# Performance work log

Measured on AMD Instinct MI355X. Metric: run time of the kernel, lower is better.

Reference implementation:

```python
import jax, jax.numpy as jnp
import numpy as np

N, E, K, IN_C, D = 50000, 800000, 3, 2, 64
RES_LAYERS = 2
EPS = 1e-5


def setup_inputs() -> dict:
    key = jax.random.key(0)
    ks = jax.random.split(key, 12)
    def w(k, shape, scale=0.05):
        return jax.random.normal(k, shape, jnp.float32) * scale
    x = jax.random.normal(ks[0], (N, IN_C), jnp.float32)
    edge_index = jax.random.randint(ks[1], (2, E), 0, N, dtype=jnp.int32)
    edge_attr = jax.random.uniform(ks[2], (E,), jnp.float32)
    # TAGConv params: first conv IN_C->D, then 2*RES_LAYERS + 1 = 5 convs D->D, each with K+1 weight mats
    tag0_w = w(ks[3], (K + 1, IN_C, D))
    tag0_b = jnp.zeros((D,), jnp.float32)
    tag_w = w(ks[4], (5, K + 1, D, D))
    tag_b = jnp.zeros((5, D), jnp.float32)
    # EdgeModel params: Lin(2D+1,D) + 2 residual blocks (Lin,ReLU,Lin)+LN + Lin(D,1)
    We0 = w(ks[5], (2 * D + 1, D)); be0 = jnp.zeros((D,), jnp.float32)
    ln0_g = jnp.ones((D,), jnp.float32); ln0_b = jnp.zeros((D,), jnp.float32)
    Wa = w(ks[6], (2, D, D)); ba = jnp.zeros((2, D), jnp.float32)
    Wb = w(ks[7], (2, D, D)); bb = jnp.zeros((2, D), jnp.float32)
    ln_g = jnp.ones((2, D), jnp.float32); ln_b = jnp.zeros((2, D), jnp.float32)
    Wf = w(ks[8], (D, 1)); bf = jnp.zeros((1,), jnp.float32)
    return dict(x=x, edge_index=edge_index, edge_attr=edge_attr,
                tag0_w=tag0_w, tag0_b=tag0_b, tag_w=tag_w, tag_b=tag_b,
                We0=We0, be0=be0, ln0_g=ln0_g, ln0_b=ln0_b,
                Wa=Wa, ba=ba, Wb=Wb, bb=bb, ln_g=ln_g, ln_b=ln_b,
                Wf=Wf, bf=bf)


def _gcn_norm(row, col, ew, n):
    # symmetric GCN normalization without self loops (PyG TAGConv default)
    deg = jnp.zeros((n,), ew.dtype).at[col].add(ew)
    deg_safe = jnp.where(deg > 0, deg, 1.0)
    dinv = jnp.where(deg > 0, jax.lax.rsqrt(deg_safe), 0.0)
    return dinv[row] * ew * dinv[col]


def _tagconv(x, row, col, norm, W, b):
    # out = sum_{k=0..K} (A_norm^k x) @ W[k] + b
    out = x @ W[0]
    h = x
    for k in range(1, K + 1):
        h = jnp.zeros(h.shape, h.dtype).at[col].add(norm[:, None] * h[row])
        out = out + h @ W[k]
    return out + b


def _inorm(x):
    # PyG InstanceNorm, single graph, affine=False: per-channel stats over nodes
    m = x.mean(0)
    v = x.var(0)
    return (x - m) * jax.lax.rsqrt(v + EPS)


def _lnorm(x, g, b):
    m = x.mean(-1, keepdims=True)
    v = x.var(-1, keepdims=True)
    return (x - m) * jax.lax.rsqrt(v + EPS) * g + b


def _forward(x, edge_index, edge_attr, tag0_w, tag0_b, tag_w, tag_b,
             We0, be0, ln0_g, ln0_b, Wa, ba, Wb, bb, ln_g, ln_b, Wf, bf):
    row, col = edge_index[0], edge_index[1]
    ew = edge_attr.reshape(-1)
    norm = _gcn_norm(row, col, ew, x.shape[0])
    # block 0: TAGConv(IN_C->D) -> InstanceNorm -> (no residual: shape change) -> ReLU
    data = jax.nn.relu(_inorm(_tagconv(x, row, col, norm, tag0_w, tag0_b)))
    # residual blocks: TAGConv -> ReLU -> TAGConv -> InstanceNorm -> +residual -> ReLU
    for i in range(RES_LAYERS):
        h = jax.nn.relu(_tagconv(data, row, col, norm, tag_w[2 * i], tag_b[2 * i]))
        h = _inorm(_tagconv(h, row, col, norm, tag_w[2 * i + 1], tag_b[2 * i + 1]))
        data = jax.nn.relu(h + data)
    # final block: TAGConv -> (no norm) -> +residual -> ReLU
    data = jax.nn.relu(_tagconv(data, row, col, norm, tag_w[4], tag_b[4]) + data)
    # edge model on gathered endpoint features + edge attr
    e = jnp.concatenate([data[row], data[col], ew[:, None]], axis=1)  # [E, 2D+1]
    h = jax.nn.relu(_lnorm(e @ We0 + be0, ln0_g, ln0_b))  # no residual (shape change)
    for j in range(2):
        h2 = jax.nn.relu(h @ Wa[j] + ba[j]) @ Wb[j] + bb[j]
        h = jax.nn.relu(_lnorm(h2, ln_g[j], ln_b[j]) + h)
    out = h @ Wf + bf  # [E, 1]
    out = (out - out.mean()) / out.std(ddof=1)
    return jnp.abs(out)


def reference(x, edge_index, edge_attr, tag0_w, tag0_b, tag_w, tag_b,
              We0, be0, ln0_g, ln0_b, Wa, ba, Wb, bb, ln_g, ln_b, Wf, bf):
    return _forward(x, edge_index, edge_attr, tag0_w, tag0_b, tag_w, tag_b,
                    We0, be0, ln0_g, ln0_b, Wa, ba, Wb, bb, ln_g, ln_b, Wf, bf)
```

## Files before the change

kernel.cpp:

```cpp
#include <hip/hip_runtime.h>

#define NN 50000
#define NE 800000
#define EPSf 1e-5f

typedef _Float16 half8 __attribute__((ext_vector_type(8)));
typedef _Float16 half4v __attribute__((ext_vector_type(4)));
typedef _Float16 half2v __attribute__((ext_vector_type(2)));
typedef float f32x4 __attribute__((ext_vector_type(4)));

#define HA_STRIDE 72
#define WT_STRIDE 136
#define WB_STRIDE 72

__global__ void deg_hist_kernel(const int* __restrict__ row, const int* __restrict__ col,
                                const float* __restrict__ ew,
                                float* __restrict__ deg, int* __restrict__ cnt) {
  int e = blockIdx.x * 256 + threadIdx.x;
  if (e >= NE) return;
  int c = col[e];
  unsafeAtomicAdd(&deg[c], ew[e]);
  atomicAdd(&cnt[c], 1);
}

__global__ void dinv_kernel(float* __restrict__ deg) {
  int n = blockIdx.x * 256 + threadIdx.x;
  if (n >= NN) return;
  float d = deg[n];
  deg[n] = d > 0.f ? rsqrtf(d) : 0.f;
}

__global__ void scan1(int* __restrict__ cnt, int* __restrict__ aux) {
  __shared__ int ls[256];
  int t = threadIdx.x, idx = blockIdx.x * 256 + t;
  int v = (idx < NN) ? cnt[idx] : 0;
  ls[t] = v;
  __syncthreads();
  for (int o = 1; o < 256; o <<= 1) {
    int u = (t >= o) ? ls[t - o] : 0;
    __syncthreads();
    ls[t] += u;
    __syncthreads();
  }
  if (idx < NN) cnt[idx] = ls[t] - v;
  if (t == 255) aux[blockIdx.x] = ls[255];
}

__global__ void scan2(int* __restrict__ aux, int nb) {
  __shared__ int ls[256];
  int t = threadIdx.x;
  int v = (t < nb) ? aux[t] : 0;
  ls[t] = v;
  __syncthreads();
  for (int o = 1; o < 256; o <<= 1) {
    int u = (t >= o) ? ls[t - o] : 0;
    __syncthreads();
    ls[t] += u;
    __syncthreads();
  }
  if (t < nb) aux[t] = ls[t] - v;
}

__global__ void scan3(int* __restrict__ cnt, const int* __restrict__ aux) {
  int idx = blockIdx.x * 256 + threadIdx.x;
  if (idx < NN) cnt[idx] += aux[idx >> 8];
}

__global__ void scatter_kernel(const int* __restrict__ row, const int* __restrict__ col,
                               const float* __restrict__ ew, const float* __restrict__ dinv,
                               int* __restrict__ rowptr, int2* __restrict__ pme) {
  int e = blockIdx.x * 256 + threadIdx.x;
  if (e >= NE) return;
  int r = row[e], c = col[e];
  float w = dinv[r] * ew[e] * dinv[c];
  int p = atomicAdd(&rowptr[c], 1);
  pme[p] = make_int2(r, __float_as_int(w));
}

__global__ void prop16(const int* __restrict__ rowptr, const int2* __restrict__ pme,
                       const _Float16* __restrict__ h, _Float16* __restrict__ hn) {
  int idx = blockIdx.x * 256 + threadIdx.x;
  if (idx >= NN * 8) return;
  int n = idx >> 3, q = idx & 7;
  int s = n ? rowptr[n - 1] : 0;
  int epos = rowptr[n];
  float a0 = 0.f, a1 = 0.f, a2 = 0.f, a3 = 0.f, a4 = 0.f, a5 = 0.f, a6 = 0.f, a7 = 0.f;
  for (int j = s; j < epos; j++) {
    int2 m = pme[j];
    float w = __int_as_float(m.y);
    half8 v = *(const half8*)&h[(size_t)m.x * 64 + q * 8];
    a0 += w * (float)v[0]; a1 += w * (float)v[1];
    a2 += w * (float)v[2]; a3 += w * (float)v[3];
    a4 += w * (float)v[4]; a5 += w * (float)v[5];
    a6 += w * (float)v[6]; a7 += w * (float)v[7];
  }
  half8 o = {(_Float16)a0, (_Float16)a1, (_Float16)a2, (_Float16)a3,
             (_Float16)a4, (_Float16)a5, (_Float16)a6, (_Float16)a7};
  *(half8*)&hn[(size_t)n * 64 + q * 8] = o;
}

__global__ void prop2_csr(const int* __restrict__ rowptr, const int2* __restrict__ pme,
                          const float* __restrict__ h, float* __restrict__ hn) {
  int n = blockIdx.x * 256 + threadIdx.x;
  if (n >= NN) return;
  int s = n ? rowptr[n - 1] : 0;
  int epos = rowptr[n];
  float a0 = 0.f, a1 = 0.f;
  for (int j = s; j < epos; j++) {
    int2 m = pme[j];
    float w = __int_as_float(m.y);
    a0 += w * h[m.x * 2 + 0];
    a1 += w * h[m.x * 2 + 1];
  }
  hn[n * 2 + 0] = a0;
  hn[n * 2 + 1] = a1;
}

__global__ void __launch_bounds__(128, 4) gemmB_mfma(
    const _Float16* __restrict__ h0, const _Float16* __restrict__ h1,
    const _Float16* __restrict__ h2, const _Float16* __restrict__ h3,
    const float* __restrict__ W,
    float* __restrict__ accG) {
  __shared__ __align__(16) _Float16 hA[128 * HA_STRIDE];
  __shared__ __align__(16) _Float16 WT[64 * WB_STRIDE];
  const int t = threadIdx.x;
  const int lane = t & 63, wv = t >> 6;
  const int a = lane & 15, g = lane >> 4;
  const int nb = blockIdx.x * 128;
  const _Float16* hs[4] = {h0, h1, h2, h3};

  f32x4 acc[4][4];
#pragma unroll
  for (int ct = 0; ct < 4; ct++)
#pragma unroll
    for (int nt = 0; nt < 4; nt++) acc[ct][nt] = (f32x4)0.f;

#pragma unroll 1
  for (int k = 0; k < 4; k++) {
    const _Float16* hk = hs[k];
    {
      size_t base = (size_t)(nb + t) * 64;
#pragma unroll
      for (int i = 0; i < 8; i++)
        *(half8*)&hA[t * HA_STRIDE + i * 8] = *(const half8*)&hk[base + i * 8];
    }
    {
      const float* Wk = W + k * 4096;
      int n = t >> 1, kb = (t & 1) * 32;
#pragma unroll
      for (int k2 = 0; k2 < 16; k2++) {
        int kk = kb + 2 * k2;
        half2v p = {(_Float16)Wk[kk * 64 + n], (_Float16)Wk[(kk + 1) * 64 + n]};
        *(half2v*)&WT[n * WB_STRIDE + kk] = p;
      }
    }
    __syncthreads();
#pragma unroll
    for (int ks = 0; ks < 2; ks++) {
      half8 wf[4], hf[4];
#pragma unroll
      for (int nt = 0; nt < 4; nt++)
        wf[nt] = *(const half8*)&WT[(nt * 16 + a) * WB_STRIDE + ks * 32 + g * 8];
#pragma unroll
      for (int ct = 0; ct < 4; ct++)
        hf[ct] = *(const half8*)&hA[(wv * 64 + ct * 16 + a) * HA_STRIDE + ks * 32 + g * 8];
#pragma unroll
      for (int ct = 0; ct < 4; ct++)
#pragma unroll
        for (int nt = 0; nt < 4; nt++)
          acc[ct][nt] = __builtin_amdgcn_mfma_f32_16x16x32_f16(wf[nt], hf[ct], acc[ct][nt], 0, 0, 0);
    }
    __syncthreads();
  }
#pragma unroll
  for (int ct = 0; ct < 4; ct++) {
    int node = nb + wv * 64 + ct * 16 + a;
    if (node < NN) {
#pragma unroll
      for (int nt = 0; nt < 4; nt++)
        *(f32x4*)&accG[(size_t)node * 64 + nt * 16 + g * 4] = acc[ct][nt];
    }
  }
}

__global__ void gemm2(const float* __restrict__ h2, const float* __restrict__ W,
                      float* __restrict__ acc, int accum) {
  int idx = blockIdx.x * 256 + threadIdx.x;
  if (idx >= NN * 16) return;
  int n = idx >> 4, q = idx & 15;
  float x0 = h2[n * 2], x1 = h2[n * 2 + 1];
  float4 w0 = ((const float4*)W)[q];
  float4 w1 = ((const float4*)W)[16 + q];
  float4 a;
  if (accum) a = ((const float4*)acc)[idx];
  else a = make_float4(0.f, 0.f, 0.f, 0.f);
  a.x += x0 * w0.x + x1 * w1.x;
  a.y += x0 * w0.y + x1 * w1.y;
  a.z += x0 * w0.z + x1 * w1.z;
  a.w += x0 * w0.w + x1 * w1.w;
  ((float4*)acc)[idx] = a;
}

__global__ void stats64(const float* __restrict__ acc, float* __restrict__ st) {
  int c = threadIdx.x & 63, g = threadIdx.x >> 6;
  float s = 0.f, ss = 0.f;
  for (int n = blockIdx.x * 4 + g; n < NN; n += gridDim.x * 4) {
    float v = acc[n * 64 + c];
    s += v; ss += v * v;
  }
  __shared__ float ls[256], lss[256];
  ls[threadIdx.x] = s; lss[threadIdx.x] = ss;
  __syncthreads();
  if (threadIdx.x < 64) {
    s = ls[threadIdx.x] + ls[threadIdx.x + 64] + ls[threadIdx.x + 128] + ls[threadIdx.x + 192];
    ss = lss[threadIdx.x] + lss[threadIdx.x + 64] + lss[threadIdx.x + 128] + lss[threadIdx.x + 192];
    unsafeAtomicAdd(&st[c], s);
    unsafeAtomicAdd(&st[64 + c], ss);
  }
}

__global__ void apply64(const float* __restrict__ acc, const float* __restrict__ bias,
                        const float* __restrict__ st, const float* __restrict__ resid,
                        float* __restrict__ out32, _Float16* __restrict__ out16,
                        int inorm, int relu) {
  int idx = blockIdx.x * 256 + threadIdx.x;
  if (idx >= NN * 16) return;
  int q = idx & 15;
  int c0 = q * 4;
  const float4 av = ((const float4*)acc)[idx];
  float v0 = av.x, v1 = av.y, v2 = av.z, v3 = av.w;
  if (inorm) {
    const float invN = 1.f / NN;
    float m0 = st[c0 + 0] * invN, m1 = st[c0 + 1] * invN;
    float m2 = st[c0 + 2] * invN, m3 = st[c0 + 3] * invN;
    float r0 = rsqrtf(st[64 + c0 + 0] * invN - m0 * m0 + EPSf);
    float r1 = rsqrtf(st[64 + c0 + 1] * invN - m1 * m1 + EPSf);
    float r2 = rsqrtf(st[64 + c0 + 2] * invN - m2 * m2 + EPSf);
    float r3 = rsqrtf(st[64 + c0 + 3] * invN - m3 * m3 + EPSf);
    v0 = (v0 - m0) * r0; v1 = (v1 - m1) * r1;
    v2 = (v2 - m2) * r2; v3 = (v3 - m3) * r3;
  } else {
    v0 += bias[c0 + 0]; v1 += bias[c0 + 1]; v2 += bias[c0 + 2]; v3 += bias[c0 + 3];
  }
  if (resid) {
    const float4 rv = ((const float4*)resid)[idx];
    v0 += rv.x; v1 += rv.y; v2 += rv.z; v3 += rv.w;
  }
  if (relu) {
    v0 = fmaxf(v0, 0.f); v1 = fmaxf(v1, 0.f);
    v2 = fmaxf(v2, 0.f); v3 = fmaxf(v3, 0.f);
  }
  if (out32) ((float4*)out32)[idx] = make_float4(v0, v1, v2, v3);
  if (out16) {
    half4v hh = {(_Float16)v0, (_Float16)v1, (_Float16)v2, (_Float16)v3};
    *(half4v*)&out16[(size_t)idx * 4] = hh;
  }
}

__device__ __forceinline__ void gemm64_step(f32x4 (&acc)[4][4],
                                            const _Float16* hAp, const _Float16* WTp,
                                            int wv, int a, int g, int koff) {
#pragma unroll
  for (int ks = 0; ks < 2; ks++) {
    half8 wf[4], hf[4];
#pragma unroll
    for (int nt = 0; nt < 4; nt++)
      wf[nt] = *(const half8*)&WTp[(nt * 16 + a) * WT_STRIDE + koff + ks * 32 + g * 8];
#pragma unroll
    for (int ct = 0; ct < 4; ct++)
      hf[ct] = *(const half8*)&hAp[(wv * 64 + ct * 16 + a) * HA_STRIDE + ks * 32 + g * 8];
#pragma unroll
    for (int ct = 0; ct < 4; ct++)
#pragma unroll
      for (int nt = 0; nt < 4; nt++)
        acc[ct][nt] = __builtin_amdgcn_mfma_f32_16x16x32_f16(wf[nt], hf[ct], acc[ct][nt], 0, 0, 0);
  }
}

__global__ void __launch_bounds__(256, 2) edge_mlp_mfma(
    const _Float16* __restrict__ dat16, const int* __restrict__ row, const int* __restrict__ col,
    const float* __restrict__ ew,
    const float* __restrict__ We0, const float* __restrict__ be0,
    const float* __restrict__ g0, const float* __restrict__ b0,
    const float* __restrict__ Wa, const float* __restrict__ ba,
    const float* __restrict__ Wb, const float* __restrict__ bb,
    const float* __restrict__ lg, const float* __restrict__ lb,
    const float* __restrict__ Wf, const float* __restrict__ bfp,
    float* __restrict__ eout) {
  __shared__ __align__(16) _Float16 hA[256 * HA_STRIDE];
  __shared__ __align__(16) _Float16 WT[64 * WT_STRIDE];
  __shared__ float sew[256];

  const int t = threadIdx.x;
  const int lane = t & 63, wv = t >> 6;
  const int a = lane & 15, g = lane >> 4;
  const int eb = blockIdx.x * 256;

  {
    int e = eb + t;
    sew[t] = ew[e];
    int r = row[e];
    const _Float16* srcp = dat16 + (size_t)r * 64;
#pragma unroll
    for (int i = 0; i < 8; i++)
      *(half8*)&hA[t * HA_STRIDE + i * 8] = *(const half8*)&srcp[i * 8];
    int n = t >> 2, kb = (t & 3) * 32;
#pragma unroll
    for (int k2 = 0; k2 < 16; k2++) {
      int k = kb + 2 * k2;
      half2v p = {(_Float16)We0[k * 64 + n], (_Float16)We0[(k + 1) * 64 + n]};
      *(half2v*)&WT[n * WT_STRIDE + k] = p;
    }
  }

  f32x4 be0v[4], w128v[4], g0v[4], b0v[4];
#pragma unroll
  for (int nt = 0; nt < 4; nt++) {
    int ch = nt * 16 + g * 4;
    be0v[nt] = *(const f32x4*)&be0[ch];
    w128v[nt] = *(const f32x4*)&We0[128 * 64 + ch];
    g0v[nt] = *(const f32x4*)&g0[ch];
    b0v[nt] = *(const f32x4*)&b0[ch];
  }

  __syncthreads();

  f32x4 acc[4][4];
#pragma unroll
  for (int ct = 0; ct < 4; ct++) {
    float we = sew[wv * 64 + ct * 16 + a];
#pragma unroll
    for (int nt = 0; nt < 4; nt++) acc[ct][nt] = be0v[nt] + we * w128v[nt];
  }
  gemm64_step(acc, hA, WT, wv, a, g, 0);
  __syncthreads();
  {
    int e = eb + t;
    int c = col[e];
    const _Float16* srcp = dat16 + (size_t)c * 64;
#pragma unroll
    for (int i = 0; i < 8; i++)
      *(half8*)&hA[t * HA_STRIDE + i * 8] = *(const half8*)&srcp[i * 8];
  }
  __syncthreads();
  gemm64_step(acc, hA, WT, wv, a, g, 64);

  f32x4 h[4][4];
#pragma unroll
  for (int ct = 0; ct < 4; ct++) {
    float s = 0.f, ss = 0.f;
#pragma unroll
    for (int nt = 0; nt < 4; nt++)
#pragma unroll
      for (int r = 0; r < 4; r++) { float v = acc[ct][nt][r]; s += v; ss += v * v; }
    s += __shfl_xor(s, 16); ss += __shfl_xor(ss, 16);
    s += __shfl_xor(s, 32); ss += __shfl_xor(ss, 32);
    float m = s * (1.f / 64);
    float is = rsqrtf(ss * (1.f / 64) - m * m + EPSf);
#pragma unroll
    for (int nt = 0; nt < 4; nt++)
#pragma unroll
      for (int r = 0; r < 4; r++)
        h[ct][nt][r] = fmaxf((acc[ct][nt][r] - m) * is * g0v[nt][r] + b0v[nt][r], 0.f);
  }
  __syncthreads();

#pragma unroll 1
  for (int j = 0; j < 2; j++) {
    {
      const float* W = Wa + j * 4096;
      int n = t >> 2, kb = (t & 3) * 16;
#pragma unroll
      for (int k2 = 0; k2 < 8; k2++) {
        int k = kb + 2 * k2;
        half2v p = {(_Float16)W[k * 64 + n], (_Float16)W[(k + 1) * 64 + n]};
        *(half2v*)&WT[n * WT_STRIDE + k] = p;
      }
    }
#pragma unroll
    for (int ct = 0; ct < 4; ct++)
#pragma unroll
      for (int nt = 0; nt < 4; nt++) {
        half4v hh = {(_Float16)h[ct][nt][0], (_Float16)h[ct][nt][1],
                     (_Float16)h[ct][nt][2], (_Float16)h[ct][nt][3]};
        *(half4v*)&hA[(wv * 64 + ct * 16 + a) * HA_STRIDE + nt * 16 + g * 4] = hh;
      }
    __syncthreads();
    f32x4 accT[4][4];
#pragma unroll
    for (int nt = 0; nt < 4; nt++) {
      f32x4 bv = *(const f32x4*)&ba[j * 64 + nt * 16 + g * 4];
#pragma unroll
      for (int ct = 0; ct < 4; ct++) accT[ct][nt] = bv;
    }
    gemm64_step(accT, hA, WT, wv, a, g, 0);
    __syncthreads();
    {
      const float* W = Wb + j * 4096;
      int n = t >> 2, kb = (t & 3) * 16;
#pragma unroll
      for (int k2 = 0; k2 < 8; k2++) {
        int k = kb + 2 * k2;
        half2v p = {(_Float16)W[k * 64 + n], (_Float16)W[(k + 1) * 64 + n]};
        *(half2v*)&WT[n * WT_STRIDE + k] = p;
      }
    }
#pragma unroll
    for (int ct = 0; ct < 4; ct++)
#pragma unroll
      for (int nt = 0; nt < 4; nt++) {
        half4v hh = {(_Float16)fmaxf(accT[ct][nt][0], 0.f), (_Float16)fmaxf(accT[ct][nt][1], 0.f),
                     (_Float16)fmaxf(accT[ct][nt][2], 0.f), (_Float16)fmaxf(accT[ct][nt][3], 0.f)};
        *(half4v*)&hA[(wv * 64 + ct * 16 + a) * HA_STRIDE + nt * 16 + g * 4] = hh;
      }
    __syncthreads();
    f32x4 accB[4][4];
#pragma unroll
    for (int nt = 0; nt < 4; nt++) {
      f32x4 bv = *(const f32x4*)&bb[j * 64 + nt * 16 + g * 4];
#pragma unroll
      for (int ct = 0; ct < 4; ct++) accB[ct][nt] = bv;
    }
    gemm64_step(accB, hA, WT, wv, a, g, 0);

    f32x4 lgv[4], lbv[4];
#pragma unroll
    for (int nt = 0; nt < 4; nt++) {
      lgv[nt] = *(const f32x4*)&lg[j * 64 + nt * 16 + g * 4];
      lbv[nt] = *(const f32x4*)&lb[j * 64 + nt * 16 + g * 4];
    }
#pragma unroll
    for (int ct = 0; ct < 4; ct++) {
      float s = 0.f, ss = 0.f;
#pragma unroll
      for (int nt = 0; nt < 4; nt++)
#pragma unroll
        for (int r = 0; r < 4; r++) { float v = accB[ct][nt][r]; s += v; ss += v * v; }
      s += __shfl_xor(s, 16); ss += __shfl_xor(ss, 16);
      s += __shfl_xor(s, 32); ss += __shfl_xor(ss, 32);
      float m = s * (1.f / 64);
      float is = rsqrtf(ss * (1.f / 64) - m * m + EPSf);
#pragma unroll
      for (int nt = 0; nt < 4; nt++)
#pragma unroll
        for (int r = 0; r < 4; r++)
          h[ct][nt][r] =
              fmaxf((accB[ct][nt][r] - m) * is * lgv[nt][r] + lbv[nt][r] + h[ct][nt][r], 0.f);
    }
    __syncthreads();
  }

  f32x4 wfv[4];
#pragma unroll
  for (int nt = 0; nt < 4; nt++) wfv[nt] = *(const f32x4*)&Wf[nt * 16 + g * 4];
  float p0 = 0.f, p1 = 0.f, p2 = 0.f, p3 = 0.f;
#pragma unroll
  for (int nt = 0; nt < 4; nt++)
#pragma unroll
    for (int r = 0; r < 4; r++) {
      p0 += h[0][nt][r] * wfv[nt][r];
      p1 += h[1][nt][r] * wfv[nt][r];
      p2 += h[2][nt][r] * wfv[nt][r];
      p3 += h[3][nt][r] * wfv[nt][r];
    }
  p0 += __shfl_xor(p0, 16); p0 += __shfl_xor(p0, 32);
  p1 += __shfl_xor(p1, 16); p1 += __shfl_xor(p1, 32);
  p2 += __shfl_xor(p2, 16); p2 += __shfl_xor(p2, 32);
  p3 += __shfl_xor(p3, 16); p3 += __shfl_xor(p3, 32);
  float sel = (g == 0) ? p0 : (g == 1) ? p1 : (g == 2) ? p2 : p3;
  eout[eb + t] = sel + bfp[0];
}

__global__ void reduce2(const float* __restrict__ v, float* __restrict__ est) {
  __shared__ float ls[256], lss[256];
  float s = 0.f, ss = 0.f;
  for (int i = blockIdx.x * 256 + threadIdx.x; i < NE; i += gridDim.x * 256) {
    float a = v[i]; s += a; ss += a * a;
  }
  ls[threadIdx.x] = s; lss[threadIdx.x] = ss;
  __syncthreads();
  for (int o = 128; o > 0; o >>= 1) {
    if (threadIdx.x < o) { ls[threadIdx.x] += ls[threadIdx.x + o]; lss[threadIdx.x] += lss[threadIdx.x + o]; }
    __syncthreads();
  }
  if (threadIdx.x == 0) {
    unsafeAtomicAdd(&est[0], ls[0]);
    unsafeAtomicAdd(&est[1], lss[0]);
  }
}

__global__ void finalize(const float* __restrict__ eo, const float* __restrict__ est,
                         float* __restrict__ out) {
  int e = blockIdx.x * 256 + threadIdx.x;
  if (e >= NE) return;
  float sum = est[0], ssq = est[1];
  float m = sum * (1.f / NE);
  float var = (ssq - sum * sum * (1.f / NE)) * (1.f / (NE - 1));
  out[e] = fabsf((eo[e] - m) * rsqrtf(var));
}

extern "C" void kernel_launch(void* const* d_in, const int* in_sizes, int n_in,
                              void* d_out, int out_size, void* d_ws, size_t ws_size,
                              hipStream_t stream) {
  const float* x   = (const float*)d_in[0];
  const int*   ei  = (const int*)d_in[1];
  const float* ew  = (const float*)d_in[2];
  const float* t0w = (const float*)d_in[3];
  const float* t0b = (const float*)d_in[4];
  const float* tw  = (const float*)d_in[5];
  const float* tb  = (const float*)d_in[6];
  const float* We0 = (const float*)d_in[7];
  const float* be0 = (const float*)d_in[8];
  const float* g0  = (const float*)d_in[9];
  const float* b0  = (const float*)d_in[10];
  const float* Wa  = (const float*)d_in[11];
  const float* ba  = (const float*)d_in[12];
  const float* Wb  = (const float*)d_in[13];
  const float* bb  = (const float*)d_in[14];
  const float* lg  = (const float*)d_in[15];
  const float* lb  = (const float*)d_in[16];
  const float* Wf  = (const float*)d_in[17];
  const float* bf  = (const float*)d_in[18];
  const int* row = ei;
  const int* col = ei + NE;

  float* ws = (float*)d_ws;
  int*       rowptr = (int*)ws;
  int2*      pme    = (int2*)(ws + 50048);
  float*     st     = ws + 1650048;
  float*     est    = st + 128;
  float*     acc    = ws + 1650240;
  float*     dat    = acc + 3200000;
  _Float16*  cur16  = (_Float16*)(ws + 8050240);
  _Float16*  mid16  = (_Float16*)(ws + 9650240);
  _Float16*  h1     = (_Float16*)(ws + 11250240);
  _Float16*  h2     = (_Float16*)(ws + 12850240);
  _Float16*  h3     = (_Float16*)(ws + 14450240);
  float*     eout   = ws + 16050240;
  float*     dinv   = ws + 11250240;
  int*       aux    = (int*)(ws + 12850240);
  float*     b2a    = ws + 14450240;
  float*     b2b    = b2a + 100096;

  dim3 blk(256);
#define GRID(n) dim3(((n) + 255) / 256)
  const int NB = (NN + 255) / 256;

  hipMemsetAsync(dinv, 0, NN * sizeof(float), stream);
  hipMemsetAsync(rowptr, 0, NN * sizeof(int), stream);
  deg_hist_kernel<<<GRID(NE), blk, 0, stream>>>(row, col, ew, dinv, rowptr);
  dinv_kernel<<<GRID(NN), blk, 0, stream>>>(dinv);
  scan1<<<dim3(NB), blk, 0, stream>>>(rowptr, aux);
  scan2<<<dim3(1), blk, 0, stream>>>(aux, NB);
  scan3<<<dim3(NB), blk, 0, stream>>>(rowptr, aux);
  scatter_kernel<<<GRID(NE), blk, 0, stream>>>(row, col, ew, dinv, rowptr, pme);

  gemm2<<<GRID(NN * 16), blk, 0, stream>>>(x, t0w, acc, 0);
  prop2_csr<<<dim3(NB), blk, 0, stream>>>(rowptr, pme, x, b2a);
  gemm2<<<GRID(NN * 16), blk, 0, stream>>>(b2a, t0w + 128, acc, 1);
  prop2_csr<<<dim3(NB), blk, 0, stream>>>(rowptr, pme, b2a, b2b);
  gemm2<<<GRID(NN * 16), blk, 0, stream>>>(b2b, t0w + 256, acc, 1);
  prop2_csr<<<dim3(NB), blk, 0, stream>>>(rowptr, pme, b2b, b2a);
  gemm2<<<GRID(NN * 16), blk, 0, stream>>>(b2a, t0w + 384, acc, 1);
  hipMemsetAsync(st, 0, 128 * sizeof(float), stream);
  stats64<<<dim3(128), blk, 0, stream>>>(acc, st);
  apply64<<<GRID(NN * 16), blk, 0, stream>>>(acc, t0b, st, nullptr, dat, cur16, 1, 1);

  const int GBB = (NN + 127) / 128;
  auto tag16 = [&](const _Float16* src, const float* W) {
    prop16<<<GRID(NN * 8), blk, 0, stream>>>(rowptr, pme, src, h1);
    prop16<<<GRID(NN * 8), blk, 0, stream>>>(rowptr, pme, h1, h2);
    prop16<<<GRID(NN * 8), blk, 0, stream>>>(rowptr, pme, h2, h3);
    gemmB_mfma<<<dim3(GBB), dim3(128), 0, stream>>>(src, h1, h2, h3, W, acc);
  };

  for (int i = 0; i < 2; i++) {
    tag16(cur16, tw + (2 * i) * 16384);
    apply64<<<GRID(NN * 16), blk, 0, stream>>>(acc, tb + (2 * i) * 64, nullptr, nullptr,
                                               nullptr, mid16, 0, 1);
    tag16(mid16, tw + (2 * i + 1) * 16384);
    hipMemsetAsync(st, 0, 128 * sizeof(float), stream);
    stats64<<<dim3(128), blk, 0, stream>>>(acc, st);
    apply64<<<GRID(NN * 16), blk, 0, stream>>>(acc, tb + (2 * i + 1) * 64, st, dat,
                                               dat, cur16, 1, 1);
  }
  tag16(cur16, tw + 4 * 16384);
  apply64<<<GRID(NN * 16), blk, 0, stream>>>(acc, tb + 4 * 64, nullptr, dat,
                                             nullptr, cur16, 0, 1);

  edge_mlp_mfma<<<GRID(NE), blk, 0, stream>>>(cur16, row, col, ew, We0, be0, g0, b0,
                                              Wa, ba, Wb, bb, lg, lb, Wf, bf, eout);
  hipMemsetAsync(est, 0, 2 * sizeof(float), stream);
  reduce2<<<dim3(1024), blk, 0, stream>>>(eout, est);
  finalize<<<GRID(NE), blk, 0, stream>>>(eout, est, (float*)d_out);
#undef GRID
}
```

Before: 886.7 us.

## Fuse TAGConv epilogues into MFMA GEMM, widen prop16, pre-convert edge-MLP weights

Bias, ReLU, residual and fp16 output are folded into the gemmB_mfma epilogue, and so are the instance-norm statistics via wave shuffles and atomics. This removes the separate apply64 and stats64 passes and one fp32 round-trip through memory. The first layer's three gemm2 launches become one gemm2B that reads all hop buffers at once. prop16 now has each thread handle 16 channels and unrolls edges by four, giving more loads in flight per thread. The edge-MLP weights are converted to transposed fp16 once in a small kernel and read straight from global memory instead of being staged into LDS in every block. The costs are global or cache weight reads inside the MFMA inner loop, more atomics on the statistics, and higher register pressure in prop16.

```diff
diff --git a/kernel.cpp b/kernel.cpp
--- a/kernel.cpp
+++ b/kernel.cpp
@@ -10,7 +10,6 @@
 typedef float f32x4 __attribute__((ext_vector_type(4)));
 
 #define HA_STRIDE 72
-#define WT_STRIDE 136
 #define WB_STRIDE 72
 
 __global__ void deg_hist_kernel(const int* __restrict__ row, const int* __restrict__ col,
@@ -77,26 +76,64 @@
   pme[p] = make_int2(r, __float_as_int(w));
 }
 
+__global__ void cvt_w(const float* __restrict__ We0, const float* __restrict__ Wa,
+                      const float* __restrict__ Wb, _Float16* __restrict__ wt) {
+  int i = blockIdx.x * 256 + threadIdx.x;
+  if (i < 8192) {
+    int n = i >> 7, k = i & 127;
+    wt[i] = (_Float16)We0[k * 64 + n];
+  } else if (i < 16384) {
+    int i2 = i - 8192, j = i2 >> 12, n = (i2 >> 6) & 63, k = i2 & 63;
+    wt[i] = (_Float16)Wa[j * 4096 + k * 64 + n];
+  } else if (i < 24576) {
+    int i2 = i - 16384, j = i2 >> 12, n = (i2 >> 6) & 63, k = i2 & 63;
+    wt[i] = (_Float16)Wb[j * 4096 + k * 64 + n];
+  }
+}
+
 __global__ void prop16(const int* __restrict__ rowptr, const int2* __restrict__ pme,
                        const _Float16* __restrict__ h, _Float16* __restrict__ hn) {
   int idx = blockIdx.x * 256 + threadIdx.x;
-  if (idx >= NN * 8) return;
-  int n = idx >> 3, q = idx & 7;
+  if (idx >= NN * 4) return;
+  int n = idx >> 2, q = idx & 3;
   int s = n ? rowptr[n - 1] : 0;
   int epos = rowptr[n];
-  float a0 = 0.f, a1 = 0.f, a2 = 0.f, a3 = 0.f, a4 = 0.f, a5 = 0.f, a6 = 0.f, a7 = 0.f;
-  for (int j = s; j < epos; j++) {
+  const _Float16* hq = h + q * 16;
+  float a[16];
+#pragma unroll
+  for (int i = 0; i < 16; i++) a[i] = 0.f;
+  int j = s;
+  for (; j + 4 <= epos; j += 4) {
+    int2 m0 = pme[j], m1 = pme[j + 1], m2 = pme[j + 2], m3 = pme[j + 3];
+    const half8* p0 = (const half8*)&hq[(size_t)m0.x * 64];
+    const half8* p1 = (const half8*)&hq[(size_t)m1.x * 64];
+    const half8* p2 = (const half8*)&hq[(size_t)m2.x * 64];
+    const half8* p3 = (const half8*)&hq[(size_t)m3.x * 64];
+    half8 u0 = p0[0], u1 = p0[1];
+    half8 u2 = p1[0], u3 = p1[1];
+    half8 u4 = p2[0], u5 = p2[1];
+    half8 u6 = p3[0], u7 = p3[1];
+    float w0 = __int_as_float(m0.y), w1 = __int_as_float(m1.y);
+    float w2 = __int_as_float(m2.y), w3 = __int_as_float(m3.y);
+#pragma unroll
+    for (int i = 0; i < 8; i++) {
+      a[i]     += w0 * (float)u0[i] + w1 * (float)u2[i] + w2 * (float)u4[i] + w3 * (float)u6[i];
+      a[i + 8] += w0 * (float)u1[i] + w1 * (float)u3[i] + w2 * (float)u5[i] + w3 * (float)u7[i];
+    }
+  }
+  for (; j < epos; j++) {
     int2 m = pme[j];
     float w = __int_as_float(m.y);
-    half8 v = *(const half8*)&h[(size_t)m.x * 64 + q * 8];
-    a0 += w * (float)v[0]; a1 += w * (float)v[1];
-    a2 += w * (float)v[2]; a3 += w * (float)v[3];
-    a4 += w * (float)v[4]; a5 += w * (float)v[5];
-    a6 += w * (float)v[6]; a7 += w * (float)v[7];
-  }
-  half8 o = {(_Float16)a0, (_Float16)a1, (_Float16)a2, (_Float16)a3,
-             (_Float16)a4, (_Float16)a5, (_Float16)a6, (_Float16)a7};
-  *(half8*)&hn[(size_t)n * 64 + q * 8] = o;
+    const half8* p = (const half8*)&hq[(size_t)m.x * 64];
+    half8 u0 = p[0], u1 = p[1];
+#pragma unroll
+    for (int i = 0; i < 8; i++) { a[i] += w * (float)u0[i]; a[i + 8] += w * (float)u1[i]; }
+  }
+  half8 o0, o1;
+#pragma unroll
+  for (int i = 0; i < 8; i++) { o0[i] = (_Float16)a[i]; o1[i] = (_Float16)a[i + 8]; }
+  *(half8*)&hn[(size_t)n * 64 + q * 16] = o0;
+  *(half8*)&hn[(size_t)n * 64 + q * 16 + 8] = o1;
 }
 
 __global__ void prop2_csr(const int* __restrict__ rowptr, const int2* __restrict__ pme,
@@ -120,7 +157,9 @@
     const _Float16* __restrict__ h0, const _Float16* __restrict__ h1,
     const _Float16* __restrict__ h2, const _Float16* __restrict__ h3,
     const float* __restrict__ W,
-    float* __restrict__ accG) {
+    float* __restrict__ accG, const float* __restrict__ bias,
+    const float* __restrict__ residF, _Float16* __restrict__ out16,
+    float* __restrict__ st) {
   __shared__ __align__(16) _Float16 hA[128 * HA_STRIDE];
   __shared__ __align__(16) _Float16 WT[64 * WB_STRIDE];
   const int t = threadIdx.x;
@@ -172,32 +211,89 @@
     }
     __syncthreads();
   }
+
+  if (st) {
+    f32x4 ps[4], pss[4];
+#pragma unroll
+    for (int nt = 0; nt < 4; nt++) { ps[nt] = (f32x4)0.f; pss[nt] = (f32x4)0.f; }
+#pragma unroll
+    for (int ct = 0; ct < 4; ct++) {
+      int node = nb + wv * 64 + ct * 16 + a;
+      if (node < NN) {
+#pragma unroll
+        for (int nt = 0; nt < 4; nt++) {
+          ps[nt] += acc[ct][nt];
+          pss[nt] += acc[ct][nt] * acc[ct][nt];
+        }
+      }
+    }
+#pragma unroll
+    for (int o = 1; o < 16; o <<= 1) {
+#pragma unroll
+      for (int nt = 0; nt < 4; nt++)
+#pragma unroll
+        for (int r = 0; r < 4; r++) {
+          ps[nt][r] += __shfl_xor(ps[nt][r], o);
+          pss[nt][r] += __shfl_xor(pss[nt][r], o);
+        }
+    }
+    if (a == 0) {
+#pragma unroll
+      for (int nt = 0; nt < 4; nt++)
+#pragma unroll
+        for (int r = 0; r < 4; r++) {
+          unsafeAtomicAdd(&st[nt * 16 + g * 4 + r], ps[nt][r]);
+          unsafeAtomicAdd(&st[64 + nt * 16 + g * 4 + r], pss[nt][r]);
+        }
+    }
+  }
+
+  f32x4 bias4[4];
+  if (bias) {
+#pragma unroll
+    for (int nt = 0; nt < 4; nt++) bias4[nt] = *(const f32x4*)&bias[nt * 16 + g * 4];
+  }
 #pragma unroll
   for (int ct = 0; ct < 4; ct++) {
     int node = nb + wv * 64 + ct * 16 + a;
-    if (node < NN) {
+    if (node >= NN) continue;
+    if (accG) {
 #pragma unroll
       for (int nt = 0; nt < 4; nt++)
         *(f32x4*)&accG[(size_t)node * 64 + nt * 16 + g * 4] = acc[ct][nt];
     }
-  }
-}
-
-__global__ void gemm2(const float* __restrict__ h2, const float* __restrict__ W,
-                      float* __restrict__ acc, int accum) {
+    if (out16) {
+#pragma unroll
+      for (int nt = 0; nt < 4; nt++) {
+        f32x4 v = acc[ct][nt] + bias4[nt];
+        if (residF) v += *(const f32x4*)&residF[(size_t)node * 64 + nt * 16 + g * 4];
+        half4v hh = {(_Float16)fmaxf(v[0], 0.f), (_Float16)fmaxf(v[1], 0.f),
+                     (_Float16)fmaxf(v[2], 0.f), (_Float16)fmaxf(v[3], 0.f)};
+        *(half4v*)&out16[(size_t)node * 64 + nt * 16 + g * 4] = hh;
+      }
+    }
+  }
+}
+
+__global__ void gemm2B(const float* __restrict__ x, const float* __restrict__ a1,
+                       const float* __restrict__ a2, const float* __restrict__ a3,
+                       const float* __restrict__ W,
+                       float* __restrict__ acc) {
   int idx = blockIdx.x * 256 + threadIdx.x;
   if (idx >= NN * 16) return;
   int n = idx >> 4, q = idx & 15;
-  float x0 = h2[n * 2], x1 = h2[n * 2 + 1];
-  float4 w0 = ((const float4*)W)[q];
-  float4 w1 = ((const float4*)W)[16 + q];
-  float4 a;
-  if (accum) a = ((const float4*)acc)[idx];
-  else a = make_float4(0.f, 0.f, 0.f, 0.f);
-  a.x += x0 * w0.x + x1 * w1.x;
-  a.y += x0 * w0.y + x1 * w1.y;
-  a.z += x0 * w0.z + x1 * w1.z;
-  a.w += x0 * w0.w + x1 * w1.w;
+  const float* srcs[4] = {x, a1, a2, a3};
+  float4 a = make_float4(0.f, 0.f, 0.f, 0.f);
+#pragma unroll
+  for (int k = 0; k < 4; k++) {
+    float x0 = srcs[k][n * 2], x1 = srcs[k][n * 2 + 1];
+    float4 w0 = ((const float4*)(W + k * 128))[q];
+    float4 w1 = ((const float4*)(W + k * 128 + 64))[q];
+    a.x += x0 * w0.x + x1 * w1.x;
+    a.y += x0 * w0.y + x1 * w1.y;
+    a.z += x0 * w0.z + x1 * w1.z;
+    a.w += x0 * w0.w + x1 * w1.w;
+  }
   ((float4*)acc)[idx] = a;
 }
 
@@ -219,37 +315,29 @@
   }
 }
 
-__global__ void apply64(const float* __restrict__ acc, const float* __restrict__ bias,
-                        const float* __restrict__ st, const float* __restrict__ resid,
-                        float* __restrict__ out32, _Float16* __restrict__ out16,
-                        int inorm, int relu) {
+__global__ void apply64(const float* __restrict__ acc, const float* __restrict__ st,
+                        const float* __restrict__ resid,
+                        float* __restrict__ out32, _Float16* __restrict__ out16) {
   int idx = blockIdx.x * 256 + threadIdx.x;
   if (idx >= NN * 16) return;
   int q = idx & 15;
   int c0 = q * 4;
   const float4 av = ((const float4*)acc)[idx];
-  float v0 = av.x, v1 = av.y, v2 = av.z, v3 = av.w;
-  if (inorm) {
-    const float invN = 1.f / NN;
-    float m0 = st[c0 + 0] * invN, m1 = st[c0 + 1] * invN;
-    float m2 = st[c0 + 2] * invN, m3 = st[c0 + 3] * invN;
-    float r0 = rsqrtf(st[64 + c0 + 0] * invN - m0 * m0 + EPSf);
-    float r1 = rsqrtf(st[64 + c0 + 1] * invN - m1 * m1 + EPSf);
-    float r2 = rsqrtf(st[64 + c0 + 2] * invN - m2 * m2 + EPSf);
-    float r3 = rsqrtf(st[64 + c0 + 3] * invN - m3 * m3 + EPSf);
-    v0 = (v0 - m0) * r0; v1 = (v1 - m1) * r1;
-    v2 = (v2 - m2) * r2; v3 = (v3 - m3) * r3;
-  } else {
-    v0 += bias[c0 + 0]; v1 += bias[c0 + 1]; v2 += bias[c0 + 2]; v3 += bias[c0 + 3];
-  }
+  const float invN = 1.f / NN;
+  float m0 = st[c0 + 0] * invN, m1 = st[c0 + 1] * invN;
+  float m2 = st[c0 + 2] * invN, m3 = st[c0 + 3] * invN;
+  float r0 = rsqrtf(st[64 + c0 + 0] * invN - m0 * m0 + EPSf);
+  float r1 = rsqrtf(st[64 + c0 + 1] * invN - m1 * m1 + EPSf);
+  float r2 = rsqrtf(st[64 + c0 + 2] * invN - m2 * m2 + EPSf);
+  float r3 = rsqrtf(st[64 + c0 + 3] * invN - m3 * m3 + EPSf);
+  float v0 = (av.x - m0) * r0, v1 = (av.y - m1) * r1;
+  float v2 = (av.z - m2) * r2, v3 = (av.w - m3) * r3;
   if (resid) {
     const float4 rv = ((const float4*)resid)[idx];
     v0 += rv.x; v1 += rv.y; v2 += rv.z; v3 += rv.w;
   }
-  if (relu) {
-    v0 = fmaxf(v0, 0.f); v1 = fmaxf(v1, 0.f);
-    v2 = fmaxf(v2, 0.f); v3 = fmaxf(v3, 0.f);
-  }
+  v0 = fmaxf(v0, 0.f); v1 = fmaxf(v1, 0.f);
+  v2 = fmaxf(v2, 0.f); v3 = fmaxf(v3, 0.f);
   if (out32) ((float4*)out32)[idx] = make_float4(v0, v1, v2, v3);
   if (out16) {
     half4v hh = {(_Float16)v0, (_Float16)v1, (_Float16)v2, (_Float16)v3};
@@ -257,15 +345,15 @@
   }
 }
 
-__device__ __forceinline__ void gemm64_step(f32x4 (&acc)[4][4],
-                                            const _Float16* hAp, const _Float16* WTp,
-                                            int wv, int a, int g, int koff) {
+__device__ __forceinline__ void gstep(f32x4 (&acc)[4][4], const _Float16* hAp,
+                                      const _Float16* __restrict__ Wg, int wstride,
+                                      int wv, int a, int g, int koff) {
 #pragma unroll
   for (int ks = 0; ks < 2; ks++) {
     half8 wf[4], hf[4];
 #pragma unroll
     for (int nt = 0; nt < 4; nt++)
-      wf[nt] = *(const half8*)&WTp[(nt * 16 + a) * WT_STRIDE + koff + ks * 32 + g * 8];
+      wf[nt] = *(const half8*)&Wg[(nt * 16 + a) * wstride + koff + ks * 32 + g * 8];
 #pragma unroll
     for (int ct = 0; ct < 4; ct++)
       hf[ct] = *(const half8*)&hAp[(wv * 64 + ct * 16 + a) * HA_STRIDE + ks * 32 + g * 8];
@@ -279,17 +367,17 @@
 
 __global__ void __launch_bounds__(256, 2) edge_mlp_mfma(
     const _Float16* __restrict__ dat16, const int* __restrict__ row, const int* __restrict__ col,
-    const float* __restrict__ ew,
+    const float* __restrict__ ew, const _Float16* __restrict__ wt16,
     const float* __restrict__ We0, const float* __restrict__ be0,
     const float* __restrict__ g0, const float* __restrict__ b0,
-    const float* __restrict__ Wa, const float* __restrict__ ba,
-    const float* __restrict__ Wb, const float* __restrict__ bb,
+    const float* __restrict__ ba, const float* __restrict__ bb,
     const float* __restrict__ lg, const float* __restrict__ lb,
     const float* __restrict__ Wf, const float* __restrict__ bfp,
     float* __restrict__ eout) {
   __shared__ __align__(16) _Float16 hA[256 * HA_STRIDE];
-  __shared__ __align__(16) _Float16 WT[64 * WT_STRIDE];
-  __shared__ float sew[256];
+  const _Float16* wt0 = wt16;
+  const _Float16* wtA = wt16 + 8192;
+  const _Float16* wtB = wt16 + 16384;
 
   const int t = threadIdx.x;
   const int lane = t & 63, wv = t >> 6;
@@ -298,19 +386,11 @@
 
   {
     int e = eb + t;
-    sew[t] = ew[e];
     int r = row[e];
     const _Float16* srcp = dat16 + (size_t)r * 64;
 #pragma unroll
     for (int i = 0; i < 8; i++)
       *(half8*)&hA[t * HA_STRIDE + i * 8] = *(const half8*)&srcp[i * 8];
-    int n = t >> 2, kb = (t & 3) * 32;
-#pragma unroll
-    for (int k2 = 0; k2 < 16; k2++) {
-      int k = kb + 2 * k2;
-      half2v p = {(_Float16)We0[k * 64 + n], (_Float16)We0[(k + 1) * 64 + n]};
-      *(half2v*)&WT[n * WT_STRIDE + k] = p;
-    }
   }
 
   f32x4 be0v[4], w128v[4], g0v[4], b0v[4];
@@ -323,16 +403,15 @@
     b0v[nt] = *(const f32x4*)&b0[ch];
   }
 
-  __syncthreads();
-
   f32x4 acc[4][4];
 #pragma unroll
   for (int ct = 0; ct < 4; ct++) {
-    float we = sew[wv * 64 + ct * 16 + a];
+    float we = ew[eb + wv * 64 + ct * 16 + a];
 #pragma unroll
     for (int nt = 0; nt < 4; nt++) acc[ct][nt] = be0v[nt] + we * w128v[nt];
   }
-  gemm64_step(acc, hA, WT, wv, a, g, 0);
+  __syncthreads();
+  gstep(acc, hA, wt0, 128, wv, a, g, 0);
   __syncthreads();
   {
     int e = eb + t;
@@ -343,7 +422,7 @@
       *(half8*)&hA[t * HA_STRIDE + i * 8] = *(const half8*)&srcp[i * 8];
   }
   __syncthreads();
-  gemm64_step(acc, hA, WT, wv, a, g, 64);
+  gstep(acc, hA, wt0, 128, wv, a, g, 64);
 
   f32x4 h[4][4];
 #pragma unroll
@@ -367,16 +446,6 @@
 
 #pragma unroll 1
   for (int j = 0; j < 2; j++) {
-    {
-      const float* W = Wa + j * 4096;
-      int n = t >> 2, kb = (t & 3) * 16;
-#pragma unroll
-      for (int k2 = 0; k2 < 8; k2++) {
-        int k = kb + 2 * k2;
-        half2v p = {(_Float16)W[k * 64 + n], (_Float16)W[(k + 1) * 64 + n]};
-        *(half2v*)&WT[n * WT_STRIDE + k] = p;
-      }
-    }
 #pragma unroll
     for (int ct = 0; ct < 4; ct++)
 #pragma unroll
@@ -393,18 +462,8 @@
 #pragma unroll
       for (int ct = 0; ct < 4; ct++) accT[ct][nt] = bv;
     }
-    gemm64_step(accT, hA, WT, wv, a, g, 0);
-    __syncthreads();
-    {
-      const float* W = Wb + j * 4096;
-      int n = t >> 2, kb = (t & 3) * 16;
-#pragma unroll
-      for (int k2 = 0; k2 < 8; k2++) {
-        int k = kb + 2 * k2;
-        half2v p = {(_Float16)W[k * 64 + n], (_Float16)W[(k + 1) * 64 + n]};
-        *(half2v*)&WT[n * WT_STRIDE + k] = p;
-      }
-    }
+    gstep(accT, hA, wtA + j * 4096, 64, wv, a, g, 0);
+    __syncthreads();
 #pragma unroll
     for (int ct = 0; ct < 4; ct++)
 #pragma unroll
@@ -421,7 +480,7 @@
 #pragma unroll
       for (int ct = 0; ct < 4; ct++) accB[ct][nt] = bv;
     }
-    gemm64_step(accB, hA, WT, wv, a, g, 0);
+    gstep(accB, hA, wtB + j * 4096, 64, wv, a, g, 0);
 
     f32x4 lgv[4], lbv[4];
 #pragma unroll
@@ -523,6 +582,7 @@
   const float* bf  = (const float*)d_in[18];
   const int* row = ei;
   const int* col = ei + NE;
+  (void)t0b;
 
   float* ws = (float*)d_ws;
   int*       rowptr = (int*)ws;
@@ -537,10 +597,12 @@
   _Float16*  h2     = (_Float16*)(ws + 12850240);
   _Float16*  h3     = (_Float16*)(ws + 14450240);
   float*     eout   = ws + 16050240;
+  _Float16*  wt16   = (_Float16*)(ws + 16850240);
   float*     dinv   = ws + 11250240;
   int*       aux    = (int*)(ws + 12850240);
   float*     b2a    = ws + 14450240;
   float*     b2b    = b2a + 100096;
+  float*     b2c    = b2b + 100096;
 
   dim3 blk(256);
 #define GRID(n) dim3(((n) + 255) / 256)
@@ -554,42 +616,42 @@
   scan2<<<dim3(1), blk, 0, stream>>>(aux, NB);
   scan3<<<dim3(NB), blk, 0, stream>>>(rowptr, aux);
   scatter_kernel<<<GRID(NE), blk, 0, stream>>>(row, col, ew, dinv, rowptr, pme);
-
-  gemm2<<<GRID(NN * 16), blk, 0, stream>>>(x, t0w, acc, 0);
+  cvt_w<<<dim3(96), blk, 0, stream>>>(We0, Wa, Wb, wt16);
+
   prop2_csr<<<dim3(NB), blk, 0, stream>>>(rowptr, pme, x, b2a);
-  gemm2<<<GRID(NN * 16), blk, 0, stream>>>(b2a, t0w + 128, acc, 1);
   prop2_csr<<<dim3(NB), blk, 0, stream>>>(rowptr, pme, b2a, b2b);
-  gemm2<<<GRID(NN * 16), blk, 0, stream>>>(b2b, t0w + 256, acc, 1);
-  prop2_csr<<<dim3(NB), blk, 0, stream>>>(rowptr, pme, b2b, b2a);
-  gemm2<<<GRID(NN * 16), blk, 0, stream>>>(b2a, t0w + 384, acc, 1);
+  prop2_csr<<<dim3(NB), blk, 0, stream>>>(rowptr, pme, b2b, b2c);
+  gemm2B<<<GRID(NN * 16), blk, 0, stream>>>(x, b2a, b2b, b2c, t0w, acc);
   hipMemsetAsync(st, 0, 128 * sizeof(float), stream);
   stats64<<<dim3(128), blk, 0, stream>>>(acc, st);
-  apply64<<<GRID(NN * 16), blk, 0, stream>>>(acc, t0b, st, nullptr, dat, cur16, 1, 1);
+  apply64<<<GRID(NN * 16), blk, 0, stream>>>(acc, st, nullptr, dat, cur16);
 
   const int GBB = (NN + 127) / 128;
-  auto tag16 = [&](const _Float16* src, const float* W) {
-    prop16<<<GRID(NN * 8), blk, 0, stream>>>(rowptr, pme, src, h1);
-    prop16<<<GRID(NN * 8), blk, 0, stream>>>(rowptr, pme, h1, h2);
-    prop16<<<GRID(NN * 8), blk, 0, stream>>>(rowptr, pme, h2, h3);
-    gemmB_mfma<<<dim3(GBB), dim3(128), 0, stream>>>(src, h1, h2, h3, W, acc);
+  auto props = [&](const _Float16* src) {
+    prop16<<<GRID(NN * 4), blk, 0, stream>>>(rowptr, pme, src, h1);
+    prop16<<<GRID(NN * 4), blk, 0, stream>>>(rowptr, pme, h1, h2);
+    prop16<<<GRID(NN * 4), blk, 0, stream>>>(rowptr, pme, h2, h3);
   };
 
   for (int i = 0; i < 2; i++) {
-    tag16(cur16, tw + (2 * i) * 16384);
-    apply64<<<GRID(NN * 16), blk, 0, stream>>>(acc, tb + (2 * i) * 64, nullptr, nullptr,
-                                               nullptr, mid16, 0, 1);
-    tag16(mid16, tw + (2 * i + 1) * 16384);
+    props(cur16);
+    gemmB_mfma<<<dim3(GBB), dim3(128), 0, stream>>>(
+        cur16, h1, h2, h3, tw + (2 * i) * 16384,
+        nullptr, tb + (2 * i) * 64, nullptr, mid16, nullptr);
+    props(mid16);
     hipMemsetAsync(st, 0, 128 * sizeof(float), stream);
-    stats64<<<dim3(128), blk, 0, stream>>>(acc, st);
-    apply64<<<GRID(NN * 16), blk, 0, stream>>>(acc, tb + (2 * i + 1) * 64, st, dat,
-                                               dat, cur16, 1, 1);
-  }
-  tag16(cur16, tw + 4 * 16384);
-  apply64<<<GRID(NN * 16), blk, 0, stream>>>(acc, tb + 4 * 64, nullptr, dat,
-                                             nullptr, cur16, 0, 1);
-
-  edge_mlp_mfma<<<GRID(NE), blk, 0, stream>>>(cur16, row, col, ew, We0, be0, g0, b0,
-                                              Wa, ba, Wb, bb, lg, lb, Wf, bf, eout);
+    gemmB_mfma<<<dim3(GBB), dim3(128), 0, stream>>>(
+        mid16, h1, h2, h3, tw + (2 * i + 1) * 16384,
+        acc, nullptr, nullptr, nullptr, st);
+    apply64<<<GRID(NN * 16), blk, 0, stream>>>(acc, st, dat, dat, cur16);
+  }
+  props(cur16);
+  gemmB_mfma<<<dim3(GBB), dim3(128), 0, stream>>>(
+      cur16, h1, h2, h3, tw + 4 * 16384,
+      nullptr, tb + 4 * 64, dat, cur16, nullptr);
+
+  edge_mlp_mfma<<<GRID(NE), blk, 0, stream>>>(cur16, row, col, ew, wt16, We0, be0, g0, b0,
+                                              ba, bb, lg, lb, Wf, bf, eout);
   hipMemsetAsync(est, 0, 2 * sizeof(float), stream);
   reduce2<<<dim3(1024), blk, 0, stream>>>(eout, est);
   finalize<<<GRID(NE), blk, 0, stream>>>(eout, est, (float*)d_out);
```

After: 920.7 us. 1.04x slower.
